# Optimization experiments

Measured on AMD Instinct MI355X. Metric: run time of the kernel, lower is better.

The kernel has to match this reference:

```python
import jax, jax.numpy as jnp
import numpy as np

B, W, LOCAL, GLOBAL = 32, 16, 64, 64
EMB, HIDDEN, OUT, NLAYERS = 256, 512, 64, 3
T = 128  # output_len


def setup_inputs() -> dict:
    key = jax.random.key(0)
    ks = jax.random.split(key, 16)
    s = 0.05
    inp = {
        "z_t": jax.random.normal(ks[0], (B, W, LOCAL), jnp.float32),
        "z_g": jax.random.normal(ks[1], (B, GLOBAL), jnp.float32),
        # embedding: Linear(local+global -> 256, bias=False), torch layout (out,in)
        "w_emb": jax.random.normal(ks[2], (EMB, LOCAL + GLOBAL), jnp.float32) * s,
        # GRU(input_size=1, hidden=256); input is all-zeros so w_ih contributes
        # nothing (only its bias b_ih matters) -> faithfully omit w_ih.
        "gru_w_hh": jax.random.normal(ks[3], (3 * EMB, EMB), jnp.float32) * s,
        "gru_b_ih": jax.random.normal(ks[4], (3 * EMB,), jnp.float32) * s,
        "gru_b_hh": jax.random.normal(ks[5], (3 * EMB,), jnp.float32) * s,
        "mlp_w1": jax.random.normal(ks[6], (HIDDEN, EMB), jnp.float32) * s,
        "mlp_b1": jax.random.normal(ks[7], (HIDDEN,), jnp.float32) * s,
        "mlp_w2": jax.random.normal(ks[8], (HIDDEN, HIDDEN), jnp.float32) * s,
        "mlp_b2": jax.random.normal(ks[9], (HIDDEN,), jnp.float32) * s,
        "mlp_w3": jax.random.normal(ks[10], (HIDDEN, HIDDEN), jnp.float32) * s,
        "mlp_b3": jax.random.normal(ks[11], (HIDDEN,), jnp.float32) * s,
        "mu_w": jax.random.normal(ks[12], (OUT, HIDDEN), jnp.float32) * s,
        "mu_b": jax.random.normal(ks[13], (OUT,), jnp.float32) * s,
        "output_len": T,
    }
    return inp


def _gru_zero_input(h0, w_hh, b_ih, b_hh, length):
    # PyTorch GRU cell with x_t == 0: input-to-hidden term reduces to b_ih.
    b_ir, b_iz, b_in = jnp.split(b_ih, 3)

    def step(h, _):
        gh = h @ w_hh.T + b_hh              # (BW, 3*EMB)
        g_r, g_z, g_n = jnp.split(gh, 3, axis=-1)
        r = jax.nn.sigmoid(b_ir + g_r)
        z = jax.nn.sigmoid(b_iz + g_z)
        n = jnp.tanh(b_in + r * g_n)
        h_new = (1.0 - z) * n + z * h
        return h_new, h_new

    _, hs = jax.lax.scan(step, h0, None, length=length)
    return hs  # (T, BW, EMB)


def reference(z_t, z_g, w_emb, gru_w_hh, gru_b_ih, gru_b_hh,
              mlp_w1, mlp_b1, mlp_w2, mlp_b2, mlp_w3, mlp_b3,
              mu_w, mu_b, output_len):
    b, nw, _ = z_t.shape
    z = jnp.concatenate(
        [z_t, jnp.broadcast_to(z_g[:, None, :], (b, nw, z_g.shape[-1]))], axis=-1)
    emb = z @ w_emb.T                        # (B, W, EMB)
    h0 = emb.reshape(b * nw, -1)             # (BW, EMB) initial hidden state

    hs = _gru_zero_input(h0, gru_w_hh, gru_b_ih, gru_b_hh, output_len)
    h_t = jnp.transpose(hs, (1, 0, 2))       # (BW, T, EMB), batch_first

    # MLP: Linear+ELU (Dropout p=0.05 is identity in eval)
    h = jax.nn.elu(h_t @ mlp_w1.T + mlp_b1)
    h = jax.nn.elu(h @ mlp_w2.T + mlp_b2)
    h = jax.nn.elu(h @ mlp_w3.T + mlp_b3)
    x_mean = h @ mu_w.T + mu_b               # (BW, T, OUT)
    return x_mean.reshape(b, nw * output_len, -1)
```

## Files before the change

### kernel.cpp

```cpp
#include <hip/hip_runtime.h>
#include <hip/hip_bf16.h>


typedef __bf16 bf16_t;
typedef __bf16 bf16x2 __attribute__((ext_vector_type(2)));
typedef __bf16 bf16x8 __attribute__((ext_vector_type(8)));
typedef float f32x4 __attribute__((ext_vector_type(4)));

#define MFMA16(a, b, c) __builtin_amdgcn_mfma_f32_16x16x32_bf16(a, b, c, 0, 0, 0)

#define EMB 256
#define TSTEPS 128
#define OUTD 64

#define HS_OFF   0u
#define H0_OFF   33554432u
#define WHH_OFF  34078720u
#define W1_OFF   34471936u
#define W2_OFF   34734080u
#define W3_OFF   35258368u
#define MUW_OFF  35782656u

__device__ __forceinline__ float rcpf(float x){ return __builtin_amdgcn_rcpf(x); }
__device__ __forceinline__ void lds_barrier() {
  asm volatile("s_waitcnt lgkmcnt(0)\n\ts_barrier" ::: "memory");
}

__global__ __launch_bounds__(256) void convert_kernel(
    const float* __restrict__ whh, const float* __restrict__ w1,
    const float* __restrict__ w2, const float* __restrict__ w3,
    const float* __restrict__ muw, char* __restrict__ ws)
{
  const int g = blockIdx.x * 256 + threadIdx.x;
  const int G = gridDim.x * 256;
  bf16_t* d;
  d = (bf16_t*)(ws + WHH_OFF); for (int i = g; i < 196608; i += G) d[i] = (bf16_t)whh[i];
  d = (bf16_t*)(ws + W1_OFF);  for (int i = g; i < 131072; i += G) d[i] = (bf16_t)w1[i];
  d = (bf16_t*)(ws + W2_OFF);  for (int i = g; i < 262144; i += G) d[i] = (bf16_t)w2[i];
  d = (bf16_t*)(ws + W3_OFF);  for (int i = g; i < 262144; i += G) d[i] = (bf16_t)w3[i];
  d = (bf16_t*)(ws + MUW_OFF); for (int i = g; i < 32768;  i += G) d[i] = (bf16_t)muw[i];
}

__global__ __launch_bounds__(256) void emb_kernel(
    const float* __restrict__ z_t, const float* __restrict__ z_g,
    const float* __restrict__ w_emb, float* __restrict__ h0)
{
  __shared__ float zrow[128];
  const int bw = blockIdx.x, tid = threadIdx.x;
  if (tid < 128)
    zrow[tid] = (tid < 64) ? z_t[bw * 64 + tid] : z_g[(bw >> 4) * 64 + (tid - 64)];
  __syncthreads();
  const float4* wp = reinterpret_cast<const float4*>(w_emb + (size_t)tid * 128);
  float s = 0.f;
#pragma unroll
  for (int k4 = 0; k4 < 32; ++k4) {
    const float4 w = wp[k4];
    s += zrow[k4 * 4 + 0] * w.x + zrow[k4 * 4 + 1] * w.y
       + zrow[k4 * 4 + 2] * w.z + zrow[k4 * 4 + 3] * w.w;
  }
  h0[(size_t)bw * 256 + tid] = s;
}

__global__ __launch_bounds__(256, 1) void gru_kernel(
    const float* __restrict__ h0, const bf16_t* __restrict__ w_hh,
    const float* __restrict__ b_ih, const float* __restrict__ b_hh,
    bf16_t* __restrict__ hs)
{
  __shared__ __align__(16) bf16_t h16[2][16][264];

  const int tid  = threadIdx.x;
  const int wv   = tid >> 6;
  const int lane = tid & 63;
  const int l15  = lane & 15;
  const int quad = lane >> 4;
  const int bw0  = blockIdx.x * 4;
  const int c0   = wv * 16 + l15;

  bf16x8 wA[8][8];
#pragma unroll
  for (int ct = 0; ct < 8; ++ct) {
    const int n = (ct >> 2) * 256 + (ct & 3) * 64 + c0;
#pragma unroll
    for (int kk = 0; kk < 8; ++kk)
      wA[ct][kk] = *reinterpret_cast<const bf16x8*>(
          w_hh + (size_t)n * 256 + kk * 32 + quad * 8);
  }
  bf16x8 wV[4][8];
#pragma unroll
  for (int j = 0; j < 4; ++j) {
    const int n = 512 + j * 64 + c0;
#pragma unroll
    for (int kk = 0; kk < 8; ++kk)
      wV[j][kk] = *reinterpret_cast<const bf16x8*>(
          w_hh + (size_t)n * 256 + kk * 32 + quad * 8);
  }

  float br[4], bz[4], bin[4], bhn[4], hm[4];
#pragma unroll
  for (int j = 0; j < 4; ++j) {
    const int c = c0 + j * 64;
    br[j]  = b_ih[c]       + b_hh[c];
    bz[j]  = b_ih[256 + c] + b_hh[256 + c];
    bin[j] = b_ih[512 + c];
    bhn[j] = b_hh[512 + c];
    hm[j]  = h0[(size_t)(bw0 + quad) * 256 + c];
  }

  {
    bf16x8 zv;
#pragma unroll
    for (int e = 0; e < 8; ++e) zv[e] = (bf16_t)0.f;
    for (int i = tid; i < 1056; i += 256)
      reinterpret_cast<bf16x8*>(h16)[i] = zv;
  }
  __syncthreads();
#pragma unroll
  for (int j = 0; j < 4; ++j)
    h16[0][quad * 4][c0 + j * 64] = (bf16_t)hm[j];
  __syncthreads();

  bf16_t* hsp = hs + ((size_t)(bw0 + quad) * TSTEPS) * EMB + c0;

#pragma unroll 1
  for (int t = 0; t < TSTEPS; ++t) {
    const bf16_t (*hr)[264] = h16[t & 1];
    bf16_t (*hw)[264] = h16[(t & 1) ^ 1];

    bf16x8 a8[8];
#pragma unroll
    for (int kk = 0; kk < 8; ++kk)
      a8[kk] = *reinterpret_cast<const bf16x8*>(&hr[l15][kk * 32 + quad * 8]);

    f32x4 acc[12] = {};
    __builtin_amdgcn_sched_barrier(0);
    asm volatile("s_nop 1" :::);

#pragma unroll
    for (int kk = 0; kk < 8; ++kk) {
#pragma unroll
      for (int ct = 0; ct < 8; ++ct)
        asm("v_mfma_f32_16x16x32_bf16 %0, %1, %2, %0"
            : "+v"(acc[ct]) : "v"(a8[kk]), "a"(wA[ct][kk]));
#pragma unroll
      for (int j = 0; j < 4; ++j)
        acc[8 + j] = MFMA16(a8[kk], wV[j][kk], acc[8 + j]);
    }

    __builtin_amdgcn_sched_barrier(0);
    asm volatile("s_nop 7\n\ts_nop 7\n\ts_nop 1" :::);
    __builtin_amdgcn_sched_barrier(0);

#pragma unroll
    for (int j = 0; j < 4; ++j) {
      const float gr = acc[j][0]     + br[j];
      const float gz = acc[4 + j][0] + bz[j];
      const float gn = acc[8 + j][0] + bhn[j];
      const float rr = rcpf(1.f + __expf(-gr));
      const float zz = rcpf(1.f + __expf(-gz));
      const float pre = bin[j] + rr * gn;
      const float nn = 1.f - 2.f * rcpf(__expf(2.f * pre) + 1.f);
      hm[j] = nn + zz * (hm[j] - nn);
      const bf16_t nh = (bf16_t)hm[j];
      hw[quad * 4][c0 + j * 64] = nh;
      hsp[(size_t)t * EMB + j * 64] = nh;
    }
    lds_barrier();
  }
}

template<int KC>
__device__ __forceinline__ void mlp_layer(
    const bf16_t* __restrict__ W, const float* __restrict__ bias,
    bf16_t (*act)[520], int wv, int l15, int quad)
{
  f32x4 acc[4][8] = {};
#pragma unroll 2
  for (int kc = 0; kc < KC; ++kc) {
#pragma unroll
    for (int kk = 0; kk < 4; ++kk) {
      bf16x8 wf[4];
#pragma unroll
      for (int ct = 0; ct < 4; ++ct)
        wf[ct] = *reinterpret_cast<const bf16x8*>(
            W + (size_t)(wv * 64 + ct * 16 + l15) * (KC * 128) + kc * 128 + kk * 32 + quad * 8);
#pragma unroll
      for (int mt = 0; mt < 8; ++mt) {
        bf16x8 a = *reinterpret_cast<const bf16x8*>(&act[mt * 16 + l15][kc * 128 + kk * 32 + quad * 8]);
#pragma unroll
        for (int ct = 0; ct < 4; ++ct)
          acc[ct][mt] = MFMA16(a, wf[ct], acc[ct][mt]);
      }
    }
  }
  __syncthreads();
#pragma unroll
  for (int ct = 0; ct < 4; ++ct) {
    const int n = wv * 64 + ct * 16 + l15;
    const float b = bias[n];
#pragma unroll
    for (int mt = 0; mt < 8; ++mt)
#pragma unroll
      for (int r = 0; r < 4; ++r) {
        float x = acc[ct][mt][r] + b;
        x = (x > 0.f) ? x : (__expf(x) - 1.f);
        act[mt * 16 + quad * 4 + r][n] = (bf16_t)x;
      }
  }
  __syncthreads();
}

__global__ __launch_bounds__(512, 2) void mlp_kernel(
    const bf16_t* __restrict__ hs,
    const bf16_t* __restrict__ w1, const float* __restrict__ b1,
    const bf16_t* __restrict__ w2, const float* __restrict__ b2,
    const bf16_t* __restrict__ w3, const float* __restrict__ b3,
    const bf16_t* __restrict__ muw, const float* __restrict__ mub,
    float* __restrict__ out)
{
  __shared__ __align__(16) bf16_t act[128][520];

  const int tid  = threadIdx.x;
  const int wv   = tid >> 6;
  const int lane = tid & 63;
  const int l15  = lane & 15;
  const int quad = lane >> 4;
  const size_t r0 = (size_t)blockIdx.x * 128;

  for (int v = tid; v < 128 * 32; v += 512) {
    const int rr = v >> 5, cc = v & 31;
    bf16x8 x = *reinterpret_cast<const bf16x8*>(hs + (r0 + rr) * EMB + cc * 8);
    *reinterpret_cast<bf16x8*>(&act[rr][cc * 8]) = x;
  }
  __syncthreads();

  mlp_layer<2>(w1, b1, act, wv, l15, quad);
  mlp_layer<4>(w2, b2, act, wv, l15, quad);
  mlp_layer<4>(w3, b3, act, wv, l15, quad);

  f32x4 macc[4] = {};
  const int n   = (wv & 3) * 16 + l15;
  const int mtb = (wv >> 2) * 4;
#pragma unroll 1
  for (int kc = 0; kc < 4; ++kc) {
#pragma unroll
    for (int kk = 0; kk < 4; ++kk) {
      bf16x8 wf = *reinterpret_cast<const bf16x8*>(
          muw + (size_t)n * 512 + kc * 128 + kk * 32 + quad * 8);
#pragma unroll
      for (int i = 0; i < 4; ++i) {
        bf16x8 a = *reinterpret_cast<const bf16x8*>(
            &act[(mtb + i) * 16 + l15][kc * 128 + kk * 32 + quad * 8]);
        macc[i] = MFMA16(a, wf, macc[i]);
      }
    }
  }
  const float mb = mub[n];
#pragma unroll
  for (int i = 0; i < 4; ++i)
#pragma unroll
    for (int r = 0; r < 4; ++r)
      out[(r0 + (mtb + i) * 16 + quad * 4 + r) * OUTD + n] = macc[i][r] + mb;
}

extern "C" void kernel_launch(void* const* d_in, const int* in_sizes, int n_in,
                              void* d_out, int out_size, void* d_ws, size_t ws_size,
                              hipStream_t stream) {
  char* ws = (char*)d_ws;

  convert_kernel<<<256, 256, 0, stream>>>(
      (const float*)d_in[3], (const float*)d_in[6], (const float*)d_in[8],
      (const float*)d_in[10], (const float*)d_in[12], ws);

  emb_kernel<<<512, 256, 0, stream>>>(
      (const float*)d_in[0], (const float*)d_in[1], (const float*)d_in[2],
      (float*)(ws + H0_OFF));

  gru_kernel<<<128, 256, 0, stream>>>(
      (const float*)(ws + H0_OFF), (const bf16_t*)(ws + WHH_OFF),
      (const float*)d_in[4], (const float*)d_in[5],
      (bf16_t*)(ws + HS_OFF));

  mlp_kernel<<<512, 512, 0, stream>>>(
      (const bf16_t*)(ws + HS_OFF),
      (const bf16_t*)(ws + W1_OFF), (const float*)d_in[7],
      (const bf16_t*)(ws + W2_OFF), (const float*)d_in[9],
      (const bf16_t*)(ws + W3_OFF), (const float*)d_in[11],
      (const bf16_t*)(ws + MUW_OFF), (const float*)d_in[13],
      (float*)d_out);
}
```

Baseline: 370.0 us.

## Pre-swizzle MLP weights into MFMA fragment order and double-buffer weight loads

The weight conversion kernel now writes the MLP and output-projection weights in a per-lane MFMA fragment layout, so each wave loads its weight fragment with one contiguous 16-byte read per lane instead of a strided row gather. The MLP layer loop is flattened and software-pipelined: the next k-step's weight fragments are prefetched into a second register buffer while the current MFMAs run, and the activation fragments are loaded from LDS in a batch. This targets global-load latency and uncoalesced weight reads in the MLP kernel. The cost is higher register pressure from the double-buffered fragments and the full unroll, which could hurt occupancy at 2 blocks per CU.

```diff
diff --git a/kernel.cpp b/kernel.cpp
--- a/kernel.cpp
+++ b/kernel.cpp
@@ -26,6 +26,24 @@
   asm volatile("s_waitcnt lgkmcnt(0)\n\ts_barrier" ::: "memory");
 }
 
+template<int KC>
+__device__ __forceinline__ void conv_frag(
+    const float* __restrict__ src, bf16_t* __restrict__ dst,
+    int NK, int g, int G)
+{
+  const int K = KC * 128;
+  for (int i = g; i < NK; i += G) {
+    const int e    = i & 7;
+    const int lane = (i >> 3) & 63;
+    const int kk   = (i >> 9) & 3;
+    const int rem  = i >> 11;
+    const int kc   = rem & (KC - 1);
+    const int nt   = rem / KC;
+    const int l15  = lane & 15, quad = lane >> 4;
+    dst[i] = (bf16_t)src[(size_t)(nt * 16 + l15) * K + kc * 128 + kk * 32 + quad * 8 + e];
+  }
+}
+
 __global__ __launch_bounds__(256) void convert_kernel(
     const float* __restrict__ whh, const float* __restrict__ w1,
     const float* __restrict__ w2, const float* __restrict__ w3,
@@ -35,10 +53,10 @@
   const int G = gridDim.x * 256;
   bf16_t* d;
   d = (bf16_t*)(ws + WHH_OFF); for (int i = g; i < 196608; i += G) d[i] = (bf16_t)whh[i];
-  d = (bf16_t*)(ws + W1_OFF);  for (int i = g; i < 131072; i += G) d[i] = (bf16_t)w1[i];
-  d = (bf16_t*)(ws + W2_OFF);  for (int i = g; i < 262144; i += G) d[i] = (bf16_t)w2[i];
-  d = (bf16_t*)(ws + W3_OFF);  for (int i = g; i < 262144; i += G) d[i] = (bf16_t)w3[i];
-  d = (bf16_t*)(ws + MUW_OFF); for (int i = g; i < 32768;  i += G) d[i] = (bf16_t)muw[i];
+  conv_frag<2>(w1,  (bf16_t*)(ws + W1_OFF),  131072, g, G);
+  conv_frag<4>(w2,  (bf16_t*)(ws + W2_OFF),  262144, g, G);
+  conv_frag<4>(w3,  (bf16_t*)(ws + W3_OFF),  262144, g, G);
+  conv_frag<4>(muw, (bf16_t*)(ws + MUW_OFF), 32768,  g, G);
 }
 
 __global__ __launch_bounds__(256) void emb_kernel(
@@ -170,28 +188,41 @@
 
 template<int KC>
 __device__ __forceinline__ void mlp_layer(
-    const bf16_t* __restrict__ W, const float* __restrict__ bias,
-    bf16_t (*act)[520], int wv, int l15, int quad)
-{
+    const bf16_t* __restrict__ Wf, const float* __restrict__ bias,
+    bf16_t (*act)[520], int wv, int lane, int l15, int quad)
+{
+  constexpr int NIT = KC * 4;
   f32x4 acc[4][8] = {};
-#pragma unroll 2
-  for (int kc = 0; kc < KC; ++kc) {
-#pragma unroll
-    for (int kk = 0; kk < 4; ++kk) {
-      bf16x8 wf[4];
+  bf16x8 wf[2][4];
+
+#pragma unroll
+  for (int ct = 0; ct < 4; ++ct)
+    wf[0][ct] = *reinterpret_cast<const bf16x8*>(
+        Wf + (((size_t)(wv * 4 + ct) * KC) << 11) + lane * 8);
+
+#pragma unroll
+  for (int it = 0; it < NIT; ++it) {
+    const int cur = it & 1, nxt = cur ^ 1;
+    if (it + 1 < NIT) {
+      const int kc1 = (it + 1) >> 2, kk1 = (it + 1) & 3;
 #pragma unroll
       for (int ct = 0; ct < 4; ++ct)
-        wf[ct] = *reinterpret_cast<const bf16x8*>(
-            W + (size_t)(wv * 64 + ct * 16 + l15) * (KC * 128) + kc * 128 + kk * 32 + quad * 8);
-#pragma unroll
-      for (int mt = 0; mt < 8; ++mt) {
-        bf16x8 a = *reinterpret_cast<const bf16x8*>(&act[mt * 16 + l15][kc * 128 + kk * 32 + quad * 8]);
-#pragma unroll
-        for (int ct = 0; ct < 4; ++ct)
-          acc[ct][mt] = MFMA16(a, wf[ct], acc[ct][mt]);
-      }
+        wf[nxt][ct] = *reinterpret_cast<const bf16x8*>(
+            Wf + ((((size_t)(wv * 4 + ct) * KC + kc1) * 4 + kk1) << 9) + lane * 8);
     }
-  }
+    const int kc = it >> 2, kk = it & 3;
+    bf16x8 a8[8];
+#pragma unroll
+    for (int mt = 0; mt < 8; ++mt)
+      a8[mt] = *reinterpret_cast<const bf16x8*>(
+          &act[mt * 16 + l15][kc * 128 + kk * 32 + quad * 8]);
+#pragma unroll
+    for (int mt = 0; mt < 8; ++mt)
+#pragma unroll
+      for (int ct = 0; ct < 4; ++ct)
+        acc[ct][mt] = MFMA16(a8[mt], wf[cur][ct], acc[ct][mt]);
+  }
+
   __syncthreads();
 #pragma unroll
   for (int ct = 0; ct < 4; ++ct) {
@@ -233,25 +264,24 @@
   }
   __syncthreads();
 
-  mlp_layer<2>(w1, b1, act, wv, l15, quad);
-  mlp_layer<4>(w2, b2, act, wv, l15, quad);
-  mlp_layer<4>(w3, b3, act, wv, l15, quad);
+  mlp_layer<2>(w1, b1, act, wv, lane, l15, quad);
+  mlp_layer<4>(w2, b2, act, wv, lane, l15, quad);
+  mlp_layer<4>(w3, b3, act, wv, lane, l15, quad);
 
   f32x4 macc[4] = {};
-  const int n   = (wv & 3) * 16 + l15;
+  const int nt  = wv & 3;
+  const int n   = nt * 16 + l15;
   const int mtb = (wv >> 2) * 4;
-#pragma unroll 1
-  for (int kc = 0; kc < 4; ++kc) {
-#pragma unroll
-    for (int kk = 0; kk < 4; ++kk) {
-      bf16x8 wf = *reinterpret_cast<const bf16x8*>(
-          muw + (size_t)n * 512 + kc * 128 + kk * 32 + quad * 8);
-#pragma unroll
-      for (int i = 0; i < 4; ++i) {
-        bf16x8 a = *reinterpret_cast<const bf16x8*>(
-            &act[(mtb + i) * 16 + l15][kc * 128 + kk * 32 + quad * 8]);
-        macc[i] = MFMA16(a, wf, macc[i]);
-      }
+#pragma unroll
+  for (int it = 0; it < 16; ++it) {
+    const int kc = it >> 2, kk = it & 3;
+    bf16x8 wfm = *reinterpret_cast<const bf16x8*>(
+        muw + ((((size_t)nt * 4 + kc) * 4 + kk) << 9) + lane * 8);
+#pragma unroll
+    for (int i = 0; i < 4; ++i) {
+      bf16x8 a = *reinterpret_cast<const bf16x8*>(
+          &act[(mtb + i) * 16 + l15][kc * 128 + kk * 32 + quad * 8]);
+      macc[i] = MFMA16(a, wfm, macc[i]);
     }
   }
   const float mb = mub[n];
```

Measured after the change: 348.5 us. 5.8% less time.
